# Kernel tuning notes

Measured on AMD Instinct MI355X. Metric: run time of the kernel, lower is better.

## Reference

```python
import jax, jax.numpy as jnp
import numpy as np

IN_F = 4096
OUT_F = 4096
N_TOK = 8192  # batch 4 * seq 2048 tokens


def setup_inputs() -> dict:
    key = jax.random.key(0)
    k1, k2, k3 = jax.random.split(key, 3)
    x = jax.random.normal(k1, (N_TOK, IN_F), dtype=jnp.float16)
    # int4-range quantized weights stored as int8, as produced by quantize_weight()
    weight_q = jax.random.randint(k2, (OUT_F, IN_F), -8, 8, dtype=jnp.int8)
    # positive per-output-channel scales (weight_max/7, clamped >= 1e-5)
    weight_scale = (jax.random.uniform(k3, (OUT_F,), dtype=jnp.float32) * 0.01 + 1e-4).astype(jnp.float16)
    return {"x": x, "weight_q": weight_q, "weight_scale": weight_scale}


def reference(x, weight_q, weight_scale):
    # per-token symmetric int4 activation quantization
    x_max = jnp.max(jnp.abs(x), axis=-1, keepdims=True)          # [N, 1]
    x_scale = jnp.maximum(x_max / jnp.float16(7.0), jnp.float16(1e-5))
    x_q = jnp.clip(jnp.round(x / x_scale), -8, 7)                # int4 values in fp16
    # fp32 GEMM emulating int4xint4 matmul
    acc = jnp.matmul(x_q.astype(jnp.float32), weight_q.astype(jnp.float32).T)  # [N, OUT]
    # dequant: (x_scale * weight_scale) is [N, OUT]; unsqueeze(0) as in original
    scale = (x_scale.astype(jnp.float32) * weight_scale.astype(jnp.float32)[None, :])[None]  # [1, N, OUT]
    out = acc * scale                                            # [1, N, OUT]
    return out.astype(x.dtype)
```

## Files before the change

### kernel.cpp

```cpp
#include <hip/hip_runtime.h>
#include <hip/hip_fp16.h>
#include <stdint.h>

#define K_DIM 4096
#define N_OUT 4096
#define BM 256
#define BN 256
#define BKB 64

typedef __attribute__((ext_vector_type(4))) int int32x4;
typedef __attribute__((ext_vector_type(16))) int int32x16;

__global__ __launch_bounds__(256) void quant_x(const float* __restrict__ x,
                                               int8_t* __restrict__ xq,
                                               float* __restrict__ xs) {
  const int row = blockIdx.x;
  const int t = threadIdx.x;
  const float4* xr = (const float4*)(x + (size_t)row * K_DIM);
  float4 v[4];
  float m = 0.f;
#pragma unroll
  for (int i = 0; i < 4; ++i) {
    v[i] = xr[t * 4 + i];
    m = fmaxf(m, fmaxf(fmaxf(fabsf(v[i].x), fabsf(v[i].y)),
                       fmaxf(fabsf(v[i].z), fabsf(v[i].w))));
  }
#pragma unroll
  for (int off = 32; off > 0; off >>= 1) m = fmaxf(m, __shfl_xor(m, off));
  __shared__ float wmax[4];
  if ((t & 63) == 0) wmax[t >> 6] = m;
  __syncthreads();
  m = fmaxf(fmaxf(wmax[0], wmax[1]), fmaxf(wmax[2], wmax[3]));

  const float eps = 1.0013580322265625e-05f;
  const float xscale = fmaxf(m / 7.0f, eps);
  if (t == 0) xs[row] = xscale;

  uint32_t p[4];
#pragma unroll
  for (int g = 0; g < 4; ++g) {
    const float* fv = (const float*)&v[g];
    uint32_t w = 0;
#pragma unroll
    for (int j = 0; j < 4; ++j) {
      float r = rintf(fv[j] / xscale);
      r = fminf(fmaxf(r, -8.f), 7.f);
      w |= ((uint32_t)(uint8_t)(int8_t)(int)r) << (8 * j);
    }
    p[g] = w;
  }
  *(uint4*)(xq + (size_t)row * K_DIM + t * 16) = *(uint4*)p;
}

__global__ __launch_bounds__(256) void pack_w(const int* __restrict__ w,
                                              uint32_t* __restrict__ wqf) {
  const int c = blockIdx.x * 256 + threadIdx.x;
  const int blk = c >> 6;
  const int l = c & 63;
  const int row = ((blk >> 7) << 5) + (l & 31);
  const int k = ((blk & 127) << 5) + ((l >> 5) << 4);
  const int4* src = (const int4*)(w + (size_t)row * K_DIM + k);
  uint32_t p[4];
#pragma unroll
  for (int g = 0; g < 4; ++g) {
    const int4 v = src[g];
    p[g] = (uint32_t)(v.x & 255) | ((uint32_t)(v.y & 255) << 8) |
           ((uint32_t)(v.z & 255) << 16) | ((uint32_t)(v.w & 255) << 24);
  }
  *(uint4*)(wqf + (size_t)c * 4) = *(uint4*)p;
}

__global__ __launch_bounds__(512, 2) void gemm_w4a4(
    const int8_t* __restrict__ xq, const uint8_t* __restrict__ wqf,
    const float* __restrict__ xs, const float* __restrict__ wscale,
    float* __restrict__ out, int M) {
  __shared__ uint8_t lds[3][32768];

  const int bid = blockIdx.x;
  const int xcd = bid & 7;
  const int i_loc = bid >> 3;
  const int mt = xcd * 4 + (i_loc & 3);
  const int nt = i_loc >> 2;
  const int tm = mt * BM;
  const int tn = nt * BN;

  const int t = threadIdx.x;
  const int l = t & 63;
  const int wv = t >> 6;
  const int wm = wv >> 2;
  const int wn = wv & 3;

  const uint8_t* gA = (const uint8_t*)xq +
                      (size_t)(tm + wv * 32 + (l & 31)) * K_DIM +
                      ((l >> 5) << 4);
  const uint8_t* gB = wqf + (size_t)(nt * 8 + wv) * 131072 + (size_t)l * 16;

  int32x16 acc[4][2] = {};

  auto stageA2 = [&](int buf, int ss) {
#pragma unroll
    for (int j = 0; j < 2; ++j) {
      __builtin_amdgcn_global_load_lds(
          (const __attribute__((address_space(1))) uint32_t*)(
              gA + ss * BKB + j * 32),
          (__attribute__((address_space(3))) uint32_t*)(
              &lds[buf][(wv * 2 + j) * 1024 + l * 16]),
          16, 0, 0);
    }
  };
  auto stageB2 = [&](int buf, int ss) {
#pragma unroll
    for (int j = 0; j < 2; ++j) {
      __builtin_amdgcn_global_load_lds(
          (const __attribute__((address_space(1))) uint32_t*)(
              gB + ((size_t)(ss * 2 + j) << 10)),
          (__attribute__((address_space(3))) uint32_t*)(
              &lds[buf][16384 + (wv * 2 + j) * 1024 + l * 16]),
          16, 0, 0);
    }
  };

#define PHASE_OPEN()                                    \
  __builtin_amdgcn_s_barrier();                         \
  asm volatile("s_waitcnt lgkmcnt(0)" ::: "memory");    \
  __builtin_amdgcn_sched_barrier(0);                    \
  __builtin_amdgcn_s_setprio(1);

#define PHASE_CLOSE()                                   \
  __builtin_amdgcn_s_setprio(0);

  const int nsteps = K_DIM / BKB;

  stageA2(0, 0);
  stageB2(0, 0);
  stageA2(1, 1);
  stageB2(1, 1);
  asm volatile("s_waitcnt vmcnt(4)" ::: "memory");
  __builtin_amdgcn_s_barrier();

  for (int s = 0; s < nsteps; ++s) {
    const int buf = s % 3;
    const int sbuf = (s + 2) % 3;
    const int ss = (s + 2) & 63;
    const uint8_t* aB = &lds[buf][(wm * 4) * 2048 + l * 16];
    const uint8_t* bB = &lds[buf][16384 + (wn * 2) * 2048 + l * 16];

    int32x4 a[2][2], b[2][2];
#pragma unroll
    for (int m = 0; m < 2; ++m)
#pragma unroll
      for (int ks = 0; ks < 2; ++ks)
        a[m][ks] = *(const int32x4*)(aB + m * 2048 + ks * 1024);
#pragma unroll
    for (int n = 0; n < 2; ++n)
#pragma unroll
      for (int ks = 0; ks < 2; ++ks)
        b[n][ks] = *(const int32x4*)(bB + n * 2048 + ks * 1024);
    stageA2(sbuf, ss);
    PHASE_OPEN()
#pragma unroll
    for (int ks = 0; ks < 2; ++ks)
#pragma unroll
      for (int m = 0; m < 2; ++m)
#pragma unroll
        for (int n = 0; n < 2; ++n)
          acc[m][n] = __builtin_amdgcn_mfma_i32_32x32x32_i8(
              a[m][ks], b[n][ks], acc[m][n], 0, 0, 0);
    PHASE_CLOSE()
    __builtin_amdgcn_s_barrier();

    int32x4 c[2][2];
#pragma unroll
    for (int m = 0; m < 2; ++m)
#pragma unroll
      for (int ks = 0; ks < 2; ++ks)
        c[m][ks] = *(const int32x4*)(aB + (2 + m) * 2048 + ks * 1024);
    stageB2(sbuf, ss);
    PHASE_OPEN()
#pragma unroll
    for (int ks = 0; ks < 2; ++ks)
#pragma unroll
      for (int m = 0; m < 2; ++m)
#pragma unroll
        for (int n = 0; n < 2; ++n)
          acc[2 + m][n] = __builtin_amdgcn_mfma_i32_32x32x32_i8(
              c[m][ks], b[n][ks], acc[2 + m][n], 0, 0, 0);
    PHASE_CLOSE()
    asm volatile("s_waitcnt vmcnt(4)" ::: "memory");
    __builtin_amdgcn_s_barrier();
  }
  asm volatile("s_waitcnt vmcnt(0)" ::: "memory");

#undef PHASE_OPEN
#undef PHASE_CLOSE

  const int colbase = tn + wn * 64;
  const int rowbase = tm + wm * 128 + 4 * (l >> 5);
#pragma unroll
  for (int m = 0; m < 4; ++m) {
#pragma unroll
    for (int n = 0; n < 2; ++n) {
      const int col = colbase + n * 32 + (l & 31);
      const float wsc = wscale[col];
#pragma unroll
      for (int j = 0; j < 16; ++j) {
        const int row = rowbase + m * 32 + (j & 3) + 8 * (j >> 2);
        const float val = (float)acc[m][n][j] * (xs[row] * wsc);
        out[(size_t)row * N_OUT + col] = __half2float(__float2half(val));
      }
    }
  }
}

extern "C" void kernel_launch(void* const* d_in, const int* in_sizes, int n_in,
                              void* d_out, int out_size, void* d_ws, size_t ws_size,
                              hipStream_t stream) {
  const float* x = (const float*)d_in[0];
  const int* w = (const int*)d_in[1];
  const float* wsc = (const float*)d_in[2];
  float* out = (float*)d_out;

  const int M = in_sizes[0] / K_DIM;

  uint8_t* ws = (uint8_t*)d_ws;
  int8_t* xq = (int8_t*)ws;
  uint8_t* wqf = ws + (size_t)M * K_DIM;
  float* xs = (float*)(ws + (size_t)M * K_DIM + (size_t)N_OUT * K_DIM);

  quant_x<<<M, 256, 0, stream>>>(x, xq, xs);
  pack_w<<<(N_OUT * K_DIM / 16) / 256, 256, 0, stream>>>(w, (uint32_t*)wqf);
  gemm_w4a4<<<(M / BM) * (N_OUT / BN), 512, 0, stream>>>(
      xq, wqf, xs, wsc, out, M);
}
```

Baseline: 194.4 us.

## Deepen GEMM LDS pipeline to four stages with register-prefetched fragments

Grows the LDS ring from three to four 32KB buffers and issues both A and B async global→LDS loads three steps ahead. It also double-buffers the MFMA operand fragments in registers: the first k-half of the next stage is read from LDS before the end-of-step barrier. This cuts the two barriers per k-step to one and overlaps LDS reads with the MFMA chains. In exchange it uses more LDS and registers. The next-stage fragment reads happen after a per-wave vmcnt wait but before the workgroup barrier, so they may read LDS that other waves have not finished filling.

```diff
diff --git a/kernel.cpp b/kernel.cpp
--- a/kernel.cpp
+++ b/kernel.cpp
@@ -74,7 +74,7 @@
     const int8_t* __restrict__ xq, const uint8_t* __restrict__ wqf,
     const float* __restrict__ xs, const float* __restrict__ wscale,
     float* __restrict__ out, int M) {
-  __shared__ uint8_t lds[3][32768];
+  __shared__ uint8_t lds[4][32768];
 
   const int bid = blockIdx.x;
   const int xcd = bid & 7;
@@ -120,79 +120,80 @@
     }
   };
 
-#define PHASE_OPEN()                                    \
-  __builtin_amdgcn_s_barrier();                         \
-  asm volatile("s_waitcnt lgkmcnt(0)" ::: "memory");    \
-  __builtin_amdgcn_sched_barrier(0);                    \
-  __builtin_amdgcn_s_setprio(1);
-
-#define PHASE_CLOSE()                                   \
-  __builtin_amdgcn_s_setprio(0);
-
   const int nsteps = K_DIM / BKB;
 
   stageA2(0, 0);
   stageB2(0, 0);
   stageA2(1, 1);
   stageB2(1, 1);
-  asm volatile("s_waitcnt vmcnt(4)" ::: "memory");
+  stageA2(2, 2);
+  stageB2(2, 2);
+  asm volatile("s_waitcnt vmcnt(6)" ::: "memory");
   __builtin_amdgcn_s_barrier();
 
+  int32x4 a0[4], b0[2], a1[4], b1[2];
+  {
+    const uint8_t* aB = &lds[0][wm * 8192 + l * 16];
+    const uint8_t* bB = &lds[0][16384 + wn * 4096 + l * 16];
+#pragma unroll
+    for (int m = 0; m < 4; ++m) a0[m] = *(const int32x4*)(aB + m * 2048);
+#pragma unroll
+    for (int n = 0; n < 2; ++n) b0[n] = *(const int32x4*)(bB + n * 2048);
+  }
+
   for (int s = 0; s < nsteps; ++s) {
-    const int buf = s % 3;
-    const int sbuf = (s + 2) % 3;
-    const int ss = (s + 2) & 63;
-    const uint8_t* aB = &lds[buf][(wm * 4) * 2048 + l * 16];
-    const uint8_t* bB = &lds[buf][16384 + (wn * 2) * 2048 + l * 16];
-
-    int32x4 a[2][2], b[2][2];
-#pragma unroll
-    for (int m = 0; m < 2; ++m)
-#pragma unroll
-      for (int ks = 0; ks < 2; ++ks)
-        a[m][ks] = *(const int32x4*)(aB + m * 2048 + ks * 1024);
+    const int buf = s & 3;
+    const int sbuf = (s + 3) & 3;
+    const int ss = (s + 3) & 63;
+    const uint8_t* aB = &lds[buf][wm * 8192 + l * 16];
+    const uint8_t* bB = &lds[buf][16384 + wn * 4096 + l * 16];
+
+#pragma unroll
+    for (int m = 0; m < 4; ++m)
+      a1[m] = *(const int32x4*)(aB + m * 2048 + 1024);
 #pragma unroll
     for (int n = 0; n < 2; ++n)
-#pragma unroll
-      for (int ks = 0; ks < 2; ++ks)
-        b[n][ks] = *(const int32x4*)(bB + n * 2048 + ks * 1024);
+      b1[n] = *(const int32x4*)(bB + n * 2048 + 1024);
     stageA2(sbuf, ss);
-    PHASE_OPEN()
-#pragma unroll
-    for (int ks = 0; ks < 2; ++ks)
-#pragma unroll
-      for (int m = 0; m < 2; ++m)
-#pragma unroll
-        for (int n = 0; n < 2; ++n)
-          acc[m][n] = __builtin_amdgcn_mfma_i32_32x32x32_i8(
-              a[m][ks], b[n][ks], acc[m][n], 0, 0, 0);
-    PHASE_CLOSE()
+    stageB2(sbuf, ss);
+
+    asm volatile("s_waitcnt lgkmcnt(6)" ::: "memory");
+    __builtin_amdgcn_sched_barrier(0);
+    __builtin_amdgcn_s_setprio(1);
+#pragma unroll
+    for (int m = 0; m < 4; ++m) {
+      acc[m][0] = __builtin_amdgcn_mfma_i32_32x32x32_i8(a0[m], b0[0],
+                                                        acc[m][0], 0, 0, 0);
+      acc[m][1] = __builtin_amdgcn_mfma_i32_32x32x32_i8(a0[m], b0[1],
+                                                        acc[m][1], 0, 0, 0);
+    }
+    __builtin_amdgcn_s_setprio(0);
+
+    asm volatile("s_waitcnt lgkmcnt(0)" ::: "memory");
+    __builtin_amdgcn_sched_barrier(0);
+    __builtin_amdgcn_s_setprio(1);
+#pragma unroll
+    for (int m = 0; m < 4; ++m) {
+      acc[m][0] = __builtin_amdgcn_mfma_i32_32x32x32_i8(a1[m], b1[0],
+                                                        acc[m][0], 0, 0, 0);
+      acc[m][1] = __builtin_amdgcn_mfma_i32_32x32x32_i8(a1[m], b1[1],
+                                                        acc[m][1], 0, 0, 0);
+    }
+    __builtin_amdgcn_s_setprio(0);
+
+    asm volatile("s_waitcnt vmcnt(6)" ::: "memory");
+    __builtin_amdgcn_sched_barrier(0);
+
+    const uint8_t* aN = &lds[(s + 1) & 3][wm * 8192 + l * 16];
+    const uint8_t* bN = &lds[(s + 1) & 3][16384 + wn * 4096 + l * 16];
+#pragma unroll
+    for (int m = 0; m < 4; ++m) a0[m] = *(const int32x4*)(aN + m * 2048);
+#pragma unroll
+    for (int n = 0; n < 2; ++n) b0[n] = *(const int32x4*)(bN + n * 2048);
+
     __builtin_amdgcn_s_barrier();
-
-    int32x4 c[2][2];
-#pragma unroll
-    for (int m = 0; m < 2; ++m)
-#pragma unroll
-      for (int ks = 0; ks < 2; ++ks)
-        c[m][ks] = *(const int32x4*)(aB + (2 + m) * 2048 + ks * 1024);
-    stageB2(sbuf, ss);
-    PHASE_OPEN()
-#pragma unroll
-    for (int ks = 0; ks < 2; ++ks)
-#pragma unroll
-      for (int m = 0; m < 2; ++m)
-#pragma unroll
-        for (int n = 0; n < 2; ++n)
-          acc[2 + m][n] = __builtin_amdgcn_mfma_i32_32x32x32_i8(
-              c[m][ks], b[n][ks], acc[2 + m][n], 0, 0, 0);
-    PHASE_CLOSE()
-    asm volatile("s_waitcnt vmcnt(4)" ::: "memory");
-    __builtin_amdgcn_s_barrier();
-  }
-  asm volatile("s_waitcnt vmcnt(0)" ::: "memory");
-
-#undef PHASE_OPEN
-#undef PHASE_CLOSE
+  }
+  asm volatile("s_waitcnt vmcnt(0) lgkmcnt(0)" ::: "memory");
 
   const int colbase = tn + wn * 64;
   const int rowbase = tm + wm * 128 + 4 * (l >> 5);
```

Measured after the change: 201.5 us. +3.7%, slower.

## Merge quant and pack kernels; use 4-deep LDS ring with unrolled loop

Applied to the files above, without the earlier changes.

Fuses the activation-quantization and weight-pack kernels into one launch, split by block index, to save a kernel launch. The GEMM main loop switches from a 3-buffer LDS ring indexed modulo 3 to a 4-buffer ring, unrolled by 4 so buffer indices become compile-time constants. This removes the modulo arithmetic and dynamic LDS addressing. It raises LDS use to 128KB per block, which likely allows only one 512-thread block per CU instead of two, undercutting the launch-bounds occupancy target.

```diff
diff --git a/kernel.cpp b/kernel.cpp
--- a/kernel.cpp
+++ b/kernel.cpp
@@ -11,70 +11,70 @@
 typedef __attribute__((ext_vector_type(4))) int int32x4;
 typedef __attribute__((ext_vector_type(16))) int int32x16;
 
-__global__ __launch_bounds__(256) void quant_x(const float* __restrict__ x,
-                                               int8_t* __restrict__ xq,
-                                               float* __restrict__ xs) {
-  const int row = blockIdx.x;
+__global__ __launch_bounds__(256) void quant_pack(
+    const float* __restrict__ x, const int* __restrict__ w,
+    int8_t* __restrict__ xq, float* __restrict__ xs,
+    uint32_t* __restrict__ wqf, int M) {
+  __shared__ float wmax[4];
   const int t = threadIdx.x;
-  const float4* xr = (const float4*)(x + (size_t)row * K_DIM);
-  float4 v[4];
-  float m = 0.f;
-#pragma unroll
-  for (int i = 0; i < 4; ++i) {
-    v[i] = xr[t * 4 + i];
-    m = fmaxf(m, fmaxf(fmaxf(fabsf(v[i].x), fabsf(v[i].y)),
-                       fmaxf(fabsf(v[i].z), fabsf(v[i].w))));
+  if ((int)blockIdx.x < M) {
+    const int row = blockIdx.x;
+    const float4* xr = (const float4*)(x + (size_t)row * K_DIM);
+    float4 v[4];
+    float m = 0.f;
+#pragma unroll
+    for (int i = 0; i < 4; ++i) {
+      v[i] = xr[t * 4 + i];
+      m = fmaxf(m, fmaxf(fmaxf(fabsf(v[i].x), fabsf(v[i].y)),
+                         fmaxf(fabsf(v[i].z), fabsf(v[i].w))));
+    }
+#pragma unroll
+    for (int off = 32; off > 0; off >>= 1) m = fmaxf(m, __shfl_xor(m, off));
+    if ((t & 63) == 0) wmax[t >> 6] = m;
+    __syncthreads();
+    m = fmaxf(fmaxf(wmax[0], wmax[1]), fmaxf(wmax[2], wmax[3]));
+
+    const float eps = 1.0013580322265625e-05f;
+    const float xscale = fmaxf(m / 7.0f, eps);
+    if (t == 0) xs[row] = xscale;
+
+    uint32_t p[4];
+#pragma unroll
+    for (int g = 0; g < 4; ++g) {
+      const float* fv = (const float*)&v[g];
+      uint32_t wd = 0;
+#pragma unroll
+      for (int j = 0; j < 4; ++j) {
+        float r = rintf(fv[j] / xscale);
+        r = fminf(fmaxf(r, -8.f), 7.f);
+        wd |= ((uint32_t)(uint8_t)(int8_t)(int)r) << (8 * j);
+      }
+      p[g] = wd;
+    }
+    *(uint4*)(xq + (size_t)row * K_DIM + t * 16) = *(uint4*)p;
+  } else {
+    const int c = (blockIdx.x - M) * 256 + t;
+    const int blk = c >> 6;
+    const int l = c & 63;
+    const int row = ((blk >> 7) << 5) + (l & 31);
+    const int k = ((blk & 127) << 5) + ((l >> 5) << 4);
+    const int4* src = (const int4*)(w + (size_t)row * K_DIM + k);
+    uint32_t p[4];
+#pragma unroll
+    for (int g = 0; g < 4; ++g) {
+      const int4 v = src[g];
+      p[g] = (uint32_t)(v.x & 255) | ((uint32_t)(v.y & 255) << 8) |
+             ((uint32_t)(v.z & 255) << 16) | ((uint32_t)(v.w & 255) << 24);
+    }
+    *(uint4*)(wqf + (size_t)c * 4) = *(uint4*)p;
   }
-#pragma unroll
-  for (int off = 32; off > 0; off >>= 1) m = fmaxf(m, __shfl_xor(m, off));
-  __shared__ float wmax[4];
-  if ((t & 63) == 0) wmax[t >> 6] = m;
-  __syncthreads();
-  m = fmaxf(fmaxf(wmax[0], wmax[1]), fmaxf(wmax[2], wmax[3]));
-
-  const float eps = 1.0013580322265625e-05f;
-  const float xscale = fmaxf(m / 7.0f, eps);
-  if (t == 0) xs[row] = xscale;
-
-  uint32_t p[4];
-#pragma unroll
-  for (int g = 0; g < 4; ++g) {
-    const float* fv = (const float*)&v[g];
-    uint32_t w = 0;
-#pragma unroll
-    for (int j = 0; j < 4; ++j) {
-      float r = rintf(fv[j] / xscale);
-      r = fminf(fmaxf(r, -8.f), 7.f);
-      w |= ((uint32_t)(uint8_t)(int8_t)(int)r) << (8 * j);
-    }
-    p[g] = w;
-  }
-  *(uint4*)(xq + (size_t)row * K_DIM + t * 16) = *(uint4*)p;
-}
-
-__global__ __launch_bounds__(256) void pack_w(const int* __restrict__ w,
-                                              uint32_t* __restrict__ wqf) {
-  const int c = blockIdx.x * 256 + threadIdx.x;
-  const int blk = c >> 6;
-  const int l = c & 63;
-  const int row = ((blk >> 7) << 5) + (l & 31);
-  const int k = ((blk & 127) << 5) + ((l >> 5) << 4);
-  const int4* src = (const int4*)(w + (size_t)row * K_DIM + k);
-  uint32_t p[4];
-#pragma unroll
-  for (int g = 0; g < 4; ++g) {
-    const int4 v = src[g];
-    p[g] = (uint32_t)(v.x & 255) | ((uint32_t)(v.y & 255) << 8) |
-           ((uint32_t)(v.z & 255) << 16) | ((uint32_t)(v.w & 255) << 24);
-  }
-  *(uint4*)(wqf + (size_t)c * 4) = *(uint4*)p;
 }
 
 __global__ __launch_bounds__(512, 2) void gemm_w4a4(
     const int8_t* __restrict__ xq, const uint8_t* __restrict__ wqf,
     const float* __restrict__ xs, const float* __restrict__ wscale,
     float* __restrict__ out, int M) {
-  __shared__ uint8_t lds[3][32768];
+  __shared__ uint8_t lds[4][32768];
 
   const int bid = blockIdx.x;
   const int xcd = bid & 7;
@@ -129,8 +129,6 @@
 #define PHASE_CLOSE()                                   \
   __builtin_amdgcn_s_setprio(0);
 
-  const int nsteps = K_DIM / BKB;
-
   stageA2(0, 0);
   stageB2(0, 0);
   stageA2(1, 1);
@@ -138,56 +136,59 @@
   asm volatile("s_waitcnt vmcnt(4)" ::: "memory");
   __builtin_amdgcn_s_barrier();
 
-  for (int s = 0; s < nsteps; ++s) {
-    const int buf = s % 3;
-    const int sbuf = (s + 2) % 3;
-    const int ss = (s + 2) & 63;
-    const uint8_t* aB = &lds[buf][(wm * 4) * 2048 + l * 16];
-    const uint8_t* bB = &lds[buf][16384 + (wn * 2) * 2048 + l * 16];
-
-    int32x4 a[2][2], b[2][2];
-#pragma unroll
-    for (int m = 0; m < 2; ++m)
+  for (int su = 0; su < 16; ++su) {
+#pragma unroll
+    for (int u = 0; u < 4; ++u) {
+      const int s = su * 4 + u;
+      const int sbuf = (u + 2) & 3;
+      const int ss = (s + 2) & 63;
+      const uint8_t* aB = &lds[u][wm * 8192 + l * 16];
+      const uint8_t* bB = &lds[u][16384 + wn * 4096 + l * 16];
+
+      int32x4 a[2][2], b[2][2];
+#pragma unroll
+      for (int m = 0; m < 2; ++m)
+#pragma unroll
+        for (int ks = 0; ks < 2; ++ks)
+          a[m][ks] = *(const int32x4*)(aB + m * 2048 + ks * 1024);
+#pragma unroll
+      for (int n = 0; n < 2; ++n)
+#pragma unroll
+        for (int ks = 0; ks < 2; ++ks)
+          b[n][ks] = *(const int32x4*)(bB + n * 2048 + ks * 1024);
+      stageA2(sbuf, ss);
+      PHASE_OPEN()
 #pragma unroll
       for (int ks = 0; ks < 2; ++ks)
-        a[m][ks] = *(const int32x4*)(aB + m * 2048 + ks * 1024);
-#pragma unroll
-    for (int n = 0; n < 2; ++n)
+#pragma unroll
+        for (int m = 0; m < 2; ++m)
+#pragma unroll
+          for (int n = 0; n < 2; ++n)
+            acc[m][n] = __builtin_amdgcn_mfma_i32_32x32x32_i8(
+                a[m][ks], b[n][ks], acc[m][n], 0, 0, 0);
+      PHASE_CLOSE()
+      __builtin_amdgcn_s_barrier();
+
+      int32x4 c[2][2];
+#pragma unroll
+      for (int m = 0; m < 2; ++m)
+#pragma unroll
+        for (int ks = 0; ks < 2; ++ks)
+          c[m][ks] = *(const int32x4*)(aB + (2 + m) * 2048 + ks * 1024);
+      stageB2(sbuf, ss);
+      PHASE_OPEN()
 #pragma unroll
       for (int ks = 0; ks < 2; ++ks)
-        b[n][ks] = *(const int32x4*)(bB + n * 2048 + ks * 1024);
-    stageA2(sbuf, ss);
-    PHASE_OPEN()
-#pragma unroll
-    for (int ks = 0; ks < 2; ++ks)
-#pragma unroll
-      for (int m = 0; m < 2; ++m)
-#pragma unroll
-        for (int n = 0; n < 2; ++n)
-          acc[m][n] = __builtin_amdgcn_mfma_i32_32x32x32_i8(
-              a[m][ks], b[n][ks], acc[m][n], 0, 0, 0);
-    PHASE_CLOSE()
-    __builtin_amdgcn_s_barrier();
-
-    int32x4 c[2][2];
-#pragma unroll
-    for (int m = 0; m < 2; ++m)
-#pragma unroll
-      for (int ks = 0; ks < 2; ++ks)
-        c[m][ks] = *(const int32x4*)(aB + (2 + m) * 2048 + ks * 1024);
-    stageB2(sbuf, ss);
-    PHASE_OPEN()
-#pragma unroll
-    for (int ks = 0; ks < 2; ++ks)
-#pragma unroll
-      for (int m = 0; m < 2; ++m)
-#pragma unroll
-        for (int n = 0; n < 2; ++n)
-          acc[2 + m][n] = __builtin_amdgcn_mfma_i32_32x32x32_i8(
-              c[m][ks], b[n][ks], acc[2 + m][n], 0, 0, 0);
-    PHASE_CLOSE()
-    asm volatile("s_waitcnt vmcnt(4)" ::: "memory");
-    __builtin_amdgcn_s_barrier();
+#pragma unroll
+        for (int m = 0; m < 2; ++m)
+#pragma unroll
+          for (int n = 0; n < 2; ++n)
+            acc[2 + m][n] = __builtin_amdgcn_mfma_i32_32x32x32_i8(
+                c[m][ks], b[n][ks], acc[2 + m][n], 0, 0, 0);
+      PHASE_CLOSE()
+      asm volatile("s_waitcnt vmcnt(4)" ::: "memory");
+      __builtin_amdgcn_s_barrier();
+    }
   }
   asm volatile("s_waitcnt vmcnt(0)" ::: "memory");
 
@@ -227,8 +228,9 @@
   uint8_t* wqf = ws + (size_t)M * K_DIM;
   float* xs = (float*)(ws + (size_t)M * K_DIM + (size_t)N_OUT * K_DIM);
 
-  quant_x<<<M, 256, 0, stream>>>(x, xq, xs);
-  pack_w<<<(N_OUT * K_DIM / 16) / 256, 256, 0, stream>>>(w, (uint32_t*)wqf);
+  const int packBlocks = N_OUT * K_DIM / 16 / 256;
+  quant_pack<<<M + packBlocks, 256, 0, stream>>>(x, w, xq, xs,
+                                                 (uint32_t*)wqf, M);
   gemm_w4a4<<<(M / BM) * (N_OUT / BN), 512, 0, stream>>>(
       xq, wqf, xs, wsc, out, M);
 }
```

After: 188.0 us. 3.3% less time.
